# Kernel tuning notes

Hardware: AMD Instinct MI355X
Metric: run time of the kernel (lower is better)

## Reference

```python
import jax, jax.numpy as jnp
import numpy as np

N = 50000   # nodes
E = 800000  # edges
B = 64      # graphs in batch
IN = 128    # in_features
HID = 64    # hidden_channels
H = 4       # head_count
C = 10      # out_classes
NEG = 0.2   # leaky relu negative slope
EPS = 1e-5  # batchnorm eps (eval mode, running mean 0 / var 1)


def _gat(x, edge_index, W, a_src, a_dst, b):
    """PyG GATConv (add_self_loops=False, concat=True), eval mode (no dropout)."""
    Hh, F = a_src.shape
    xW = (x @ W).reshape(-1, Hh, F)                       # [N,H,F]
    src, dst = edge_index[0], edge_index[1]
    e = (jnp.einsum('nhf,hf->nh', xW, a_src)[src]
         + jnp.einsum('nhf,hf->nh', xW, a_dst)[dst])      # [E,H]
    e = jnp.where(e > 0, e, NEG * e)                      # leaky relu
    m = jax.ops.segment_max(e, dst, num_segments=N)       # per-dst max
    m = jnp.where(jnp.isfinite(m), m, 0.0)
    p = jnp.exp(e - m[dst])
    denom = jax.ops.segment_sum(p, dst, num_segments=N)
    alpha = p / jnp.maximum(denom[dst], 1e-16)            # edge softmax over dst
    out = jax.ops.segment_sum(alpha[:, :, None] * xW[src], dst, num_segments=N)
    return out.reshape(-1, Hh * F) + b


def _bn_relu(y, g, be):
    # BatchNorm1d in eval mode with running_mean=0, running_var=1, then ReLU
    return jax.nn.relu(g * y / jnp.sqrt(1.0 + EPS) + be)


def setup_inputs():
    key = jax.random.key(0)
    ks = jax.random.split(key, 24)
    s = lambda k, shape: (jax.random.normal(k, shape, jnp.float32) * 0.05)
    z = lambda shape: jnp.zeros(shape, jnp.float32)
    o = lambda shape: jnp.ones(shape, jnp.float32)
    return {
        'acc_flag': 0,
        'x': jax.random.normal(ks[0], (N, IN), jnp.float32),
        'edge_index': jax.random.randint(ks[1], (2, E), 0, N),
        'batch': jnp.sort(jax.random.randint(ks[2], (N,), 0, B)),
        # layer 1: GATConv(IN -> HID, heads=H, concat)
        'W1': s(ks[3], (IN, H * HID)), 'a_src1': s(ks[4], (H, HID)), 'a_dst1': s(ks[5], (H, HID)), 'b1': z((H * HID,)),
        # proj: GATConv(H*HID -> HID, heads=1) + BN
        'W2': s(ks[6], (H * HID, HID)), 'a_src2': s(ks[7], (1, HID)), 'a_dst2': s(ks[8], (1, HID)), 'b2': z((HID,)), 'g2': o((HID,)), 'be2': z((HID,)),
        # block 1
        'W3': s(ks[9], (HID, HID)), 'a_src3': s(ks[10], (1, HID)), 'a_dst3': s(ks[11], (1, HID)), 'b3': z((HID,)), 'g3': o((HID,)), 'be3': z((HID,)),
        # block 2
        'W4': s(ks[12], (HID, HID)), 'a_src4': s(ks[13], (1, HID)), 'a_dst4': s(ks[14], (1, HID)), 'b4': z((HID,)), 'g4': o((HID,)), 'be4': z((HID,)),
        # MLP head
        'Wh1': s(ks[15], (HID, 128)), 'bh1': z((128,)),
        'Wh2': s(ks[16], (128, C)), 'bh2': z((C,)),
    }


def reference(acc_flag, x, edge_index, batch,
              W1, a_src1, a_dst1, b1,
              W2, a_src2, a_dst2, b2, g2, be2,
              W3, a_src3, a_dst3, b3, g3, be3,
              W4, a_src4, a_dst4, b4, g4, be4,
              Wh1, bh1, Wh2, bh2):
    # hardware GAT layer + ReLU (relu applied twice in original -> idempotent)
    x1 = jax.nn.relu(_gat(x, edge_index, W1, a_src1, a_dst1, b1))   # [N, H*HID]
    # projection block: residual base is zeros (shape mismatch H*HID vs HID)
    h = _bn_relu(_gat(x1, edge_index, W2, a_src2, a_dst2, b2), g2, be2)
    # residual blocks (shapes match -> x + relu(bn(y)))
    h = h + _bn_relu(_gat(h, edge_index, W3, a_src3, a_dst3, b3), g3, be3)
    h = h + _bn_relu(_gat(h, edge_index, W4, a_src4, a_dst4, b4), g4, be4)
    # global mean pool over graphs
    pooled = jax.ops.segment_sum(h, batch, num_segments=B)
    cnt = jnp.maximum(jax.ops.segment_sum(jnp.ones((N,), h.dtype), batch, num_segments=B), 1.0)
    hp = pooled / cnt[:, None]                                      # [B, HID]
    # MLP head
    return jax.nn.relu(hp @ Wh1 + bh1) @ Wh2 + bh2                  # [B, C]
```

## Files before the change

### kernel.cpp

```cpp
#include <hip/hip_runtime.h>

#define N_NODES 50000
#define N_EDGES 800000
#define N_GRAPHS 64
#define NEG_SLOPE 0.2f
#define BN_RSQ 0.9999950000374997f
#define NB_SCAN ((N_NODES + 255) / 256)

typedef __bf16 bf16x8 __attribute__((ext_vector_type(8)));
typedef float floatx4 __attribute__((ext_vector_type(4)));

__device__ __forceinline__ float lrelu(float v) { return v > 0.0f ? v : NEG_SLOPE * v; }

__device__ __forceinline__ float b2f(unsigned short u) {
    return __uint_as_float(((unsigned int)u) << 16);
}
__device__ __forceinline__ unsigned short f2b(float f) {
    unsigned int u = __float_as_uint(f);
    return (unsigned short)((u + 0x7fffu + ((u >> 16) & 1u)) >> 16);
}
__device__ __forceinline__ float blo(unsigned int d) { return __uint_as_float(d << 16); }
__device__ __forceinline__ float bhi(unsigned int d) { return __uint_as_float(d & 0xffff0000u); }

__global__ void k_prep(const int* __restrict__ ei, int* __restrict__ deg,
                       const float* __restrict__ W1, const float* __restrict__ W2,
                       const float* __restrict__ W3, const float* __restrict__ W4,
                       unsigned short* __restrict__ Wt1, unsigned short* __restrict__ Wt2,
                       unsigned short* __restrict__ Wt3, unsigned short* __restrict__ Wt4) {
    int i = blockIdx.x * 256 + threadIdx.x;
    if (i < 32768) {
        int k = i >> 8, n = i & 255;
        Wt1[n * 128 + k] = f2b(W1[i]);
    } else if (i < 49152) {
        int j = i - 32768;
        int k = j >> 6, n = j & 63;
        Wt2[n * 256 + k] = f2b(W2[j]);
    } else if (i < 53248) {
        int j = i - 49152;
        int k = j >> 6, n = j & 63;
        Wt3[n * 64 + k] = f2b(W3[j]);
    } else if (i < 57344) {
        int j = i - 53248;
        int k = j >> 6, n = j & 63;
        Wt4[n * 64 + k] = f2b(W4[j]);
    }
    if (i < N_EDGES) atomicAdd(&deg[ei[N_EDGES + i]], 1);
}

__global__ __launch_bounds__(256) void k_offs(const int* __restrict__ deg, int* __restrict__ offs,
                                              int* __restrict__ total, const int* __restrict__ batch,
                                              int* __restrict__ bounds, int* __restrict__ bh) {
    __shared__ int lh[64];
    if (threadIdx.x < 64) lh[threadIdx.x] = 0;
    __syncthreads();
    if (blockIdx.x == 0 && threadIdx.x <= N_GRAPHS) {
        int g = threadIdx.x;
        int lo = 0, hi = N_NODES;
        while (lo < hi) {
            int mid = (lo + hi) >> 1;
            if (batch[mid] < g) lo = mid + 1; else hi = mid;
        }
        bounds[g] = lo;
    }
    int i = blockIdx.x * blockDim.x + threadIdx.x;
    int lane = threadIdx.x & 63;
    int v = (i < N_NODES) ? deg[i] : 0;
    int incl = v;
    for (int o = 1; o < 64; o <<= 1) {
        int t = __shfl_up(incl, o);
        if (lane >= o) incl += t;
    }
    int wtot = __shfl(incl, 63);
    int base = 0;
    if (lane == 0) base = atomicAdd(total, wtot);
    base = __shfl(base, 0);
    if (i < N_NODES) {
        offs[i] = base + incl - v;
        atomicAdd(&lh[63 - min(v, 63)], 1);
    }
    __syncthreads();
    if (threadIdx.x < 64) bh[blockIdx.x * 64 + threadIdx.x] = lh[threadIdx.x];
}

__global__ __launch_bounds__(256) void k_pscan(const int* __restrict__ bh, int* __restrict__ bb) {
    __shared__ int partial[4][64];
    __shared__ int bbase[64];
    const int tid = threadIdx.x;
    const int b = tid & 63, q = tid >> 6;
    const int per = (NB_SCAN + 3) / 4;
    const int k0 = q * per, k1 = min(k0 + per, NB_SCAN);
    int s = 0;
    for (int k = k0; k < k1; ++k) s += bh[k * 64 + b];
    partial[q][b] = s;
    __syncthreads();
    if (tid < 64) {
        int tot = partial[0][tid] + partial[1][tid] + partial[2][tid] + partial[3][tid];
        int incl = tot;
        for (int o = 1; o < 64; o <<= 1) {
            int t2 = __shfl_up(incl, o);
            if (tid >= o) incl += t2;
        }
        bbase[tid] = incl - tot;
    }
    __syncthreads();
    int run = bbase[b];
    for (int q2 = 0; q2 < q; ++q2) run += partial[q2][b];
    for (int k = k0; k < k1; ++k) {
        bb[k * 64 + b] = run;
        run += bh[k * 64 + b];
    }
}

__global__ __launch_bounds__(256) void k_fillperm(const int* __restrict__ ei,
                                                  const int* __restrict__ offs,
                                                  int* __restrict__ cur, int* __restrict__ csr_src,
                                                  const int* __restrict__ deg,
                                                  const int* __restrict__ bb,
                                                  int* __restrict__ perm) {
    __shared__ int lcnt[64];
    if (blockIdx.x < NB_SCAN) {
        if (threadIdx.x < 64) lcnt[threadIdx.x] = 0;
        __syncthreads();
        int i = blockIdx.x * 256 + threadIdx.x;
        if (i < N_NODES) {
            int b = 63 - min(deg[i], 63);
            int r = atomicAdd(&lcnt[b], 1);
            perm[bb[blockIdx.x * 64 + b] + r] = i;
        }
    }
    int e = blockIdx.x * 256 + threadIdx.x;
    if (e < N_EDGES) {
        int d = ei[N_EDGES + e];
        int pos = offs[d] + atomicAdd(&cur[d], 1);
        csr_src[pos] = ei[e];
    }
}

template <int K, int N, int HEADS, bool AF32>
__global__ __launch_bounds__(256) void k_mgemm(const void* __restrict__ Ap,
                                               const unsigned short* __restrict__ Bt,
                                               const float* __restrict__ asrc,
                                               const float* __restrict__ adst,
                                               unsigned short* __restrict__ out,
                                               float* __restrict__ es,
                                               float* __restrict__ ed, int rows) {
    constexpr int LDP = K + 8;
    __shared__ unsigned short As[64 * LDP];
    const int tid = threadIdx.x;
    const int r0 = blockIdx.x * 64;
    if (AF32) {
        const float* A = (const float*)Ap;
        for (int i = tid; i < 16 * K; i += 256) {
            int r = i / (K / 4), c4 = i % (K / 4);
            int row = r0 + r;
            float4 v = (row < rows) ? *(const float4*)&A[(size_t)row * K + c4 * 4]
                                    : make_float4(0.f, 0.f, 0.f, 0.f);
            ushort4 u;
            u.x = f2b(v.x); u.y = f2b(v.y); u.z = f2b(v.z); u.w = f2b(v.w);
            *(ushort4*)&As[r * LDP + c4 * 4] = u;
        }
    } else {
        const unsigned short* A = (const unsigned short*)Ap;
        for (int i = tid; i < 8 * K; i += 256) {
            int r = i / (K / 8), c8 = i % (K / 8);
            int row = r0 + r;
            uint4 v;
            if (row < rows) v = *(const uint4*)&A[(size_t)row * K + c8 * 8];
            else { v.x = v.y = v.z = v.w = 0; }
            *(uint4*)&As[r * LDP + c8 * 8] = v;
        }
    }
    __syncthreads();
    const int w = tid >> 6, lane = tid & 63;
    const int quad = lane >> 4, l16 = lane & 15;
    const int gr0 = r0 + w * 16 + quad * 4;
    bf16x8 afrag[K / 32];
#pragma unroll
    for (int kk = 0; kk < K / 32; ++kk)
        afrag[kk] = *(const bf16x8*)&As[(w * 16 + l16) * LDP + kk * 32 + quad * 8];
    float sacc[4] = {0.f, 0.f, 0.f, 0.f};
    float dacc[4] = {0.f, 0.f, 0.f, 0.f};
#pragma unroll 1
    for (int ct = 0; ct < N / 16; ++ct) {
        floatx4 acc = {0.f, 0.f, 0.f, 0.f};
#pragma unroll
        for (int kk = 0; kk < K / 32; ++kk) {
            const bf16x8 bfrag =
                *(const bf16x8*)&Bt[(size_t)(ct * 16 + l16) * K + kk * 32 + quad * 8];
            acc = __builtin_amdgcn_mfma_f32_16x16x32_bf16(afrag[kk], bfrag, acc, 0, 0, 0);
        }
        const int gc = ct * 16 + l16;
        const int hh = gc >> 6;
        const int f = gc & 63;
        const float as = asrc[hh * 64 + f];
        const float ad = adst[hh * 64 + f];
#pragma unroll
        for (int rg = 0; rg < 4; ++rg) {
            sacc[rg] = fmaf(acc[rg], as, sacc[rg]);
            dacc[rg] = fmaf(acc[rg], ad, dacc[rg]);
        }
#pragma unroll
        for (int rg = 0; rg < 4; ++rg) {
            int gr = gr0 + rg;
            if (gr < rows) out[(size_t)gr * N + gc] = f2b(acc[rg]);
        }
        if ((ct & 3) == 3) {
#pragma unroll
            for (int rg = 0; rg < 4; ++rg) {
                float s = sacc[rg], d = dacc[rg];
                for (int o = 1; o < 16; o <<= 1) {
                    s += __shfl_xor(s, o);
                    d += __shfl_xor(d, o);
                }
                if (l16 == 0) {
                    int gr = gr0 + rg;
                    if (gr < rows) {
                        es[(size_t)gr * HEADS + hh] = s;
                        ed[(size_t)gr * HEADS + hh] = d;
                    }
                }
                sacc[rg] = 0.f;
                dacc[rg] = 0.f;
            }
        }
    }
}

__global__ __launch_bounds__(256) void k_gat1(
    const unsigned short* __restrict__ xW, const float* __restrict__ es, const float* __restrict__ ed,
    const int* __restrict__ offs, const int* __restrict__ deg, const int* __restrict__ csr,
    const int* __restrict__ perm, const float* __restrict__ bias, unsigned short* __restrict__ out) {
    __shared__ float ps[4][4 * 68];
    __shared__ int sbuf[4][64];
    const int wv = threadIdx.x >> 6;
    const int lane = threadIdx.x & 63;
    const int grp = lane >> 4, t = lane & 15;
    const int h = t >> 2;
    const int g0 = blockIdx.x * 16 + wv * 4 + grp;
    if (g0 >= N_NODES / 2) return;
    const int cb = t * 16;

#pragma unroll 1
    for (int half = 0; half < 2; ++half) {
        const int pidx = half ? (N_NODES - 1 - g0) : g0;
        const int n = perm[pidx];
        const int off = offs[n];
        const int dg = deg[n];
        const float4 edv = *(const float4*)&ed[n * 4];

        float acc[16];
#pragma unroll
        for (int k = 0; k < 16; ++k) acc[k] = 0.f;
        float dsum = 0.f;

        for (int base = 0; base < dg; base += 16) {
            const int idx = base + t;
            int s_l = 0;
            float p0 = 0.f, p1 = 0.f, p2 = 0.f, p3 = 0.f;
            if (idx < dg) {
                s_l = csr[off + idx];
                const float4 ev = *(const float4*)&es[s_l * 4];
                p0 = __expf(lrelu(ev.x + edv.x));
                p1 = __expf(lrelu(ev.y + edv.y));
                p2 = __expf(lrelu(ev.z + edv.z));
                p3 = __expf(lrelu(ev.w + edv.w));
            }
            *(float4*)&ps[wv][grp * 68 + t * 4] = make_float4(p0, p1, p2, p3);
            sbuf[wv][grp * 16 + t] = s_l;
            const int cnt = min(16, dg - base);
            const int cntR = (cnt + 3) & ~3;
            for (int j = 0; j < cntR; j += 4) {
                const float pa = ps[wv][grp * 68 + (j + 0) * 4 + h];
                const float pb = ps[wv][grp * 68 + (j + 1) * 4 + h];
                const float pc = ps[wv][grp * 68 + (j + 2) * 4 + h];
                const float pd = ps[wv][grp * 68 + (j + 3) * 4 + h];
                const int sa = sbuf[wv][grp * 16 + j + 0];
                const int sb = sbuf[wv][grp * 16 + j + 1];
                const int sc = sbuf[wv][grp * 16 + j + 2];
                const int sd = sbuf[wv][grp * 16 + j + 3];
                const uint4 a0 = *(const uint4*)&xW[(size_t)sa * 256 + cb];
                const uint4 a1 = *(const uint4*)&xW[(size_t)sa * 256 + cb + 8];
                const uint4 b0 = *(const uint4*)&xW[(size_t)sb * 256 + cb];
                const uint4 b1 = *(const uint4*)&xW[(size_t)sb * 256 + cb + 8];
                const uint4 c0 = *(const uint4*)&xW[(size_t)sc * 256 + cb];
                const uint4 c1 = *(const uint4*)&xW[(size_t)sc * 256 + cb + 8];
                const uint4 d0 = *(const uint4*)&xW[(size_t)sd * 256 + cb];
                const uint4 d1 = *(const uint4*)&xW[(size_t)sd * 256 + cb + 8];
                dsum += (pa + pb) + (pc + pd);
                acc[0]  = fmaf(pa, blo(a0.x), acc[0]);
                acc[1]  = fmaf(pa, bhi(a0.x), acc[1]);
                acc[2]  = fmaf(pa, blo(a0.y), acc[2]);
                acc[3]  = fmaf(pa, bhi(a0.y), acc[3]);
                acc[4]  = fmaf(pa, blo(a0.z), acc[4]);
                acc[5]  = fmaf(pa, bhi(a0.z), acc[5]);
                acc[6]  = fmaf(pa, blo(a0.w), acc[6]);
                acc[7]  = fmaf(pa, bhi(a0.w), acc[7]);
                acc[8]  = fmaf(pa, blo(a1.x), acc[8]);
                acc[9]  = fmaf(pa, bhi(a1.x), acc[9]);
                acc[10] = fmaf(pa, blo(a1.y), acc[10]);
                acc[11] = fmaf(pa, bhi(a1.y), acc[11]);
                acc[12] = fmaf(pa, blo(a1.z), acc[12]);
                acc[13] = fmaf(pa, bhi(a1.z), acc[13]);
                acc[14] = fmaf(pa, blo(a1.w), acc[14]);
                acc[15] = fmaf(pa, bhi(a1.w), acc[15]);
                acc[0]  = fmaf(pb, blo(b0.x), acc[0]);
                acc[1]  = fmaf(pb, bhi(b0.x), acc[1]);
                acc[2]  = fmaf(pb, blo(b0.y), acc[2]);
                acc[3]  = fmaf(pb, bhi(b0.y), acc[3]);
                acc[4]  = fmaf(pb, blo(b0.z), acc[4]);
                acc[5]  = fmaf(pb, bhi(b0.z), acc[5]);
                acc[6]  = fmaf(pb, blo(b0.w), acc[6]);
                acc[7]  = fmaf(pb, bhi(b0.w), acc[7]);
                acc[8]  = fmaf(pb, blo(b1.x), acc[8]);
                acc[9]  = fmaf(pb, bhi(b1.x), acc[9]);
                acc[10] = fmaf(pb, blo(b1.y), acc[10]);
                acc[11] = fmaf(pb, bhi(b1.y), acc[11]);
                acc[12] = fmaf(pb, blo(b1.z), acc[12]);
                acc[13] = fmaf(pb, bhi(b1.z), acc[13]);
                acc[14] = fmaf(pb, blo(b1.w), acc[14]);
                acc[15] = fmaf(pb, bhi(b1.w), acc[15]);
                acc[0]  = fmaf(pc, blo(c0.x), acc[0]);
                acc[1]  = fmaf(pc, bhi(c0.x), acc[1]);
                acc[2]  = fmaf(pc, blo(c0.y), acc[2]);
                acc[3]  = fmaf(pc, bhi(c0.y), acc[3]);
                acc[4]  = fmaf(pc, blo(c0.z), acc[4]);
                acc[5]  = fmaf(pc, bhi(c0.z), acc[5]);
                acc[6]  = fmaf(pc, blo(c0.w), acc[6]);
                acc[7]  = fmaf(pc, bhi(c0.w), acc[7]);
                acc[8]  = fmaf(pc, blo(c1.x), acc[8]);
                acc[9]  = fmaf(pc, bhi(c1.x), acc[9]);
                acc[10] = fmaf(pc, blo(c1.y), acc[10]);
                acc[11] = fmaf(pc, bhi(c1.y), acc[11]);
                acc[12] = fmaf(pc, blo(c1.z), acc[12]);
                acc[13] = fmaf(pc, bhi(c1.z), acc[13]);
                acc[14] = fmaf(pc, blo(c1.w), acc[14]);
                acc[15] = fmaf(pc, bhi(c1.w), acc[15]);
                acc[0]  = fmaf(pd, blo(d0.x), acc[0]);
                acc[1]  = fmaf(pd, bhi(d0.x), acc[1]);
                acc[2]  = fmaf(pd, blo(d0.y), acc[2]);
                acc[3]  = fmaf(pd, bhi(d0.y), acc[3]);
                acc[4]  = fmaf(pd, blo(d0.z), acc[4]);
                acc[5]  = fmaf(pd, bhi(d0.z), acc[5]);
                acc[6]  = fmaf(pd, blo(d0.w), acc[6]);
                acc[7]  = fmaf(pd, bhi(d0.w), acc[7]);
                acc[8]  = fmaf(pd, blo(d1.x), acc[8]);
                acc[9]  = fmaf(pd, bhi(d1.x), acc[9]);
                acc[10] = fmaf(pd, blo(d1.y), acc[10]);
                acc[11] = fmaf(pd, bhi(d1.y), acc[11]);
                acc[12] = fmaf(pd, blo(d1.z), acc[12]);
                acc[13] = fmaf(pd, bhi(d1.z), acc[13]);
                acc[14] = fmaf(pd, blo(d1.w), acc[14]);
                acc[15] = fmaf(pd, bhi(d1.w), acc[15]);
            }
        }
        const float inv = 1.0f / fmaxf(dsum, 1e-16f);
#pragma unroll
        for (int k4 = 0; k4 < 16; k4 += 4) {
            const int c = cb + k4;
            const float4 bv = *(const float4*)&bias[c];
            ushort4 o4;
            o4.x = f2b(fmaxf(fmaf(acc[k4 + 0], inv, bv.x), 0.f));
            o4.y = f2b(fmaxf(fmaf(acc[k4 + 1], inv, bv.y), 0.f));
            o4.z = f2b(fmaxf(fmaf(acc[k4 + 2], inv, bv.z), 0.f));
            o4.w = f2b(fmaxf(fmaf(acc[k4 + 3], inv, bv.w), 0.f));
            *(ushort4*)&out[(size_t)n * 256 + c] = o4;
        }
    }
}

template <bool RES>
__global__ __launch_bounds__(256) void k_gatL(
    const unsigned short* __restrict__ xW, const float* __restrict__ es, const float* __restrict__ ed,
    const int* __restrict__ offs, const int* __restrict__ deg, const int* __restrict__ csr,
    const int* __restrict__ perm, const float* __restrict__ bias, const float* __restrict__ gam,
    const float* __restrict__ bet, float* __restrict__ h, unsigned short* __restrict__ hb) {
    __shared__ float ps[4][64];
    __shared__ int sbuf[4][64];
    const int wv = threadIdx.x >> 6;
    const int lane = threadIdx.x & 63;
    const int grp = lane >> 3, t = lane & 7;
    const int pidx = blockIdx.x * 32 + wv * 8 + grp;
    if (pidx >= N_NODES) return;
    const int n = perm[pidx];
    const int off = offs[n];
    const int dg = deg[n];
    const float edn = ed[n];
    const int cb = t * 8;

    float acc[8];
#pragma unroll
    for (int k = 0; k < 8; ++k) acc[k] = 0.f;
    float dsum = 0.f;

    for (int base = 0; base < dg; base += 8) {
        const int idx = base + t;
        int s_l = 0;
        float p_l = 0.f;
        if (idx < dg) {
            s_l = csr[off + idx];
            p_l = __expf(lrelu(es[s_l] + edn));
        }
        ps[wv][grp * 8 + t] = p_l;
        sbuf[wv][grp * 8 + t] = s_l;
        float pp[8];
        int ss[8];
#pragma unroll
        for (int q = 0; q < 8; ++q) {
            pp[q] = ps[wv][grp * 8 + q];
            ss[q] = sbuf[wv][grp * 8 + q];
        }
        uint4 u[8];
#pragma unroll
        for (int q = 0; q < 8; ++q) u[q] = *(const uint4*)&xW[(size_t)ss[q] * 64 + cb];
#pragma unroll
        for (int q = 0; q < 8; ++q) {
            dsum += pp[q];
            acc[0] = fmaf(pp[q], blo(u[q].x), acc[0]);
            acc[1] = fmaf(pp[q], bhi(u[q].x), acc[1]);
            acc[2] = fmaf(pp[q], blo(u[q].y), acc[2]);
            acc[3] = fmaf(pp[q], bhi(u[q].y), acc[3]);
            acc[4] = fmaf(pp[q], blo(u[q].z), acc[4]);
            acc[5] = fmaf(pp[q], bhi(u[q].z), acc[5]);
            acc[6] = fmaf(pp[q], blo(u[q].w), acc[6]);
            acc[7] = fmaf(pp[q], bhi(u[q].w), acc[7]);
        }
    }
    const float inv = 1.0f / fmaxf(dsum, 1e-16f);
    float hn[8];
#pragma unroll
    for (int k = 0; k < 8; ++k) {
        const int c = cb + k;
        const float y = fmaf(acc[k], inv, bias[c]);
        const float z = fmaxf(fmaf(gam[c] * y, BN_RSQ, bet[c]), 0.f);
        hn[k] = RES ? h[(size_t)n * 64 + c] + z : z;
    }
    *(float4*)&h[(size_t)n * 64 + cb] = make_float4(hn[0], hn[1], hn[2], hn[3]);
    *(float4*)&h[(size_t)n * 64 + cb + 4] = make_float4(hn[4], hn[5], hn[6], hn[7]);
    ushort4 u0, u1;
    u0.x = f2b(hn[0]); u0.y = f2b(hn[1]); u0.z = f2b(hn[2]); u0.w = f2b(hn[3]);
    u1.x = f2b(hn[4]); u1.y = f2b(hn[5]); u1.z = f2b(hn[6]); u1.w = f2b(hn[7]);
    *(ushort4*)&hb[(size_t)n * 64 + cb] = u0;
    *(ushort4*)&hb[(size_t)n * 64 + cb + 4] = u1;
}

__global__ __launch_bounds__(256) void k_pool2(const float* __restrict__ h,
                                               const int* __restrict__ bounds,
                                               float* __restrict__ hp) {
    __shared__ float part[4][64];
    const int g = blockIdx.x;
    const int lane = threadIdx.x & 63;
    const int wid = threadIdx.x >> 6;
    const int s = bounds[g], e = bounds[g + 1];
    float acc = 0.f;
    for (int n = s + wid; n < e; n += 4) acc += h[n * 64 + lane];
    part[wid][lane] = acc;
    __syncthreads();
    if (wid == 0) {
        float v = part[0][lane] + part[1][lane] + part[2][lane] + part[3][lane];
        hp[g * 64 + lane] = v / fmaxf((float)(e - s), 1.0f);
    }
}

__global__ __launch_bounds__(256) void k_head(const float* __restrict__ hpg,
                                              const float* __restrict__ Wh1,
                                              const float* __restrict__ bh1,
                                              const float* __restrict__ Wh2,
                                              const float* __restrict__ bh2,
                                              float* __restrict__ out) {
    __shared__ float hp[64 * 64];
    __shared__ float t1[64 * 128];
    const int tid = threadIdx.x;
    for (int i = tid; i < 64 * 64; i += 256) hp[i] = hpg[i];
    __syncthreads();
    for (int i = tid; i < 64 * 128; i += 256) {
        int g = i >> 7, j = i & 127;
        float s = bh1[j];
        for (int k = 0; k < 64; ++k) s = fmaf(hp[g * 64 + k], Wh1[k * 128 + j], s);
        t1[i] = fmaxf(s, 0.f);
    }
    __syncthreads();
    for (int i = tid; i < 640; i += 256) {
        int g = i / 10, j = i - g * 10;
        float s = bh2[j];
        for (int k = 0; k < 128; ++k) s = fmaf(t1[g * 128 + k], Wh2[k * 10 + j], s);
        out[i] = s;
    }
}

extern "C" void kernel_launch(void* const* d_in, const int* in_sizes, int n_in,
                              void* d_out, int out_size, void* d_ws, size_t ws_size,
                              hipStream_t stream) {
    const float* x = (const float*)d_in[1];
    const int* ei = (const int*)d_in[2];
    const int* batch = (const int*)d_in[3];
    const float* W1 = (const float*)d_in[4];
    const float* a_src1 = (const float*)d_in[5];
    const float* a_dst1 = (const float*)d_in[6];
    const float* b1 = (const float*)d_in[7];
    const float* W2 = (const float*)d_in[8];
    const float* a_src2 = (const float*)d_in[9];
    const float* a_dst2 = (const float*)d_in[10];
    const float* b2 = (const float*)d_in[11];
    const float* g2 = (const float*)d_in[12];
    const float* be2 = (const float*)d_in[13];
    const float* W3 = (const float*)d_in[14];
    const float* a_src3 = (const float*)d_in[15];
    const float* a_dst3 = (const float*)d_in[16];
    const float* b3 = (const float*)d_in[17];
    const float* g3 = (const float*)d_in[18];
    const float* be3 = (const float*)d_in[19];
    const float* W4 = (const float*)d_in[20];
    const float* a_src4 = (const float*)d_in[21];
    const float* a_dst4 = (const float*)d_in[22];
    const float* b4 = (const float*)d_in[23];
    const float* g4 = (const float*)d_in[24];
    const float* be4 = (const float*)d_in[25];
    const float* Wh1 = (const float*)d_in[26];
    const float* bh1 = (const float*)d_in[27];
    const float* Wh2 = (const float*)d_in[28];
    const float* bh2 = (const float*)d_in[29];
    float* out = (float*)d_out;

    char* p = (char*)d_ws;
    auto alloc = [&](size_t bytes) {
        void* r = (void*)p;
        p += (bytes + 255) & ~(size_t)255;
        return r;
    };
    unsigned short* bufA = (unsigned short*)alloc((size_t)N_NODES * 256 * 2);
    unsigned short* x1b = (unsigned short*)alloc((size_t)N_NODES * 256 * 2);
    float* h = (float*)alloc((size_t)N_NODES * 64 * 4);
    unsigned short* hb = (unsigned short*)alloc((size_t)N_NODES * 64 * 2);
    float* es1 = (float*)alloc((size_t)N_NODES * 4 * 4);
    float* ed1 = (float*)alloc((size_t)N_NODES * 4 * 4);
    float* esL = (float*)alloc((size_t)N_NODES * 4);
    float* edL = (float*)alloc((size_t)N_NODES * 4);
    int* offs = (int*)alloc((size_t)N_NODES * 4);
    int* csr = (int*)alloc((size_t)N_EDGES * 4);
    int* perm = (int*)alloc((size_t)N_NODES * 4);
    int* bounds = (int*)alloc((size_t)(N_GRAPHS + 1) * 4);
    int* bh_hist = (int*)alloc((size_t)NB_SCAN * 64 * 4);
    int* bb = (int*)alloc((size_t)NB_SCAN * 64 * 4);
    float* hpool = (float*)alloc((size_t)N_GRAPHS * 64 * 4);
    unsigned short* Wt1 = (unsigned short*)alloc((size_t)128 * 256 * 2);
    unsigned short* Wt2 = (unsigned short*)alloc((size_t)256 * 64 * 2);
    unsigned short* Wt3 = (unsigned short*)alloc((size_t)64 * 64 * 2);
    unsigned short* Wt4 = (unsigned short*)alloc((size_t)64 * 64 * 2);
    char* z0 = p;
    int* deg = (int*)alloc((size_t)N_NODES * 4);
    int* cur = (int*)alloc((size_t)N_NODES * 4);
    int* total = (int*)alloc(256);
    size_t zbytes = (size_t)(p - z0);
    hipMemsetAsync(z0, 0, zbytes, stream);

    const int edgeBlocks = (N_EDGES + 255) / 256;
    const int mgemmBlocks = (N_NODES + 63) / 64;
    const int gat1Blocks = (N_NODES / 2 + 15) / 16;
    const int gatLBlocks = (N_NODES + 31) / 32;

    k_prep<<<edgeBlocks, 256, 0, stream>>>(ei, deg, W1, W2, W3, W4, Wt1, Wt2, Wt3, Wt4);

    k_offs<<<NB_SCAN, 256, 0, stream>>>(deg, offs, total, batch, bounds, bh_hist);
    k_pscan<<<1, 256, 0, stream>>>(bh_hist, bb);
    k_fillperm<<<edgeBlocks, 256, 0, stream>>>(ei, offs, cur, csr, deg, bb, perm);

    k_mgemm<128, 256, 4, true><<<mgemmBlocks, 256, 0, stream>>>(x, Wt1, a_src1, a_dst1,
                                                                bufA, es1, ed1, N_NODES);
    k_gat1<<<gat1Blocks, 256, 0, stream>>>(bufA, es1, ed1, offs, deg, csr, perm, b1, x1b);

    k_mgemm<256, 64, 1, false><<<mgemmBlocks, 256, 0, stream>>>(x1b, Wt2, a_src2, a_dst2,
                                                                bufA, esL, edL, N_NODES);
    k_gatL<false><<<gatLBlocks, 256, 0, stream>>>(bufA, esL, edL, offs, deg, csr, perm, b2, g2, be2, h, hb);

    k_mgemm<64, 64, 1, false><<<mgemmBlocks, 256, 0, stream>>>(hb, Wt3, a_src3, a_dst3,
                                                               bufA, esL, edL, N_NODES);
    k_gatL<true><<<gatLBlocks, 256, 0, stream>>>(bufA, esL, edL, offs, deg, csr, perm, b3, g3, be3, h, hb);

    k_mgemm<64, 64, 1, false><<<mgemmBlocks, 256, 0, stream>>>(hb, Wt4, a_src4, a_dst4,
                                                               bufA, esL, edL, N_NODES);
    k_gatL<true><<<gatLBlocks, 256, 0, stream>>>(bufA, esL, edL, offs, deg, csr, perm, b4, g4, be4, h, hb);

    k_pool2<<<N_GRAPHS, 256, 0, stream>>>(h, bounds, hpool);
    k_head<<<1, 256, 0, stream>>>(hpool, Wh1, bh1, Wh2, bh2, out);
}
```

Baseline: 523.6 us.

## Fuse next layer's projection GEMM and attention logits into GAT aggregation kernels

Each GAT aggregation kernel now multiplies its 16 or 32 output rows by the next layer's weight matrix with MFMA and writes the projected bf16 features plus the per-node attention logits. This removes the separate k_mgemm launches and the global round trip of x1 (256 bf16 per node) and the bf16 copy of h. Each layer gets its own logit and feature buffers so no kernel reads what it writes. k_gat1 also drops its two-nodes-per-group balancing loop in favour of one node per group, which may reduce load balancing across the degree-sorted perm and adds shared memory plus barriers per block.

```diff
diff --git a/kernel.cpp b/kernel.cpp
--- a/kernel.cpp
+++ b/kernel.cpp
@@ -226,154 +226,335 @@
     }
 }
 
-__global__ __launch_bounds__(256) void k_gat1(
+__global__ __launch_bounds__(256) void k_gat1f(
     const unsigned short* __restrict__ xW, const float* __restrict__ es, const float* __restrict__ ed,
     const int* __restrict__ offs, const int* __restrict__ deg, const int* __restrict__ csr,
-    const int* __restrict__ perm, const float* __restrict__ bias, unsigned short* __restrict__ out) {
+    const int* __restrict__ perm, const float* __restrict__ bias,
+    const unsigned short* __restrict__ Bt2, const float* __restrict__ as2,
+    const float* __restrict__ ad2, unsigned short* __restrict__ outW,
+    float* __restrict__ es2o, float* __restrict__ ed2o) {
     __shared__ float ps[4][4 * 68];
     __shared__ int sbuf[4][64];
+    __shared__ unsigned short As2[16 * 264];
+    __shared__ int nbuf[16];
+    __shared__ float sds[4][16], sdd[4][16];
     const int wv = threadIdx.x >> 6;
     const int lane = threadIdx.x & 63;
     const int grp = lane >> 4, t = lane & 15;
     const int h = t >> 2;
-    const int g0 = blockIdx.x * 16 + wv * 4 + grp;
-    if (g0 >= N_NODES / 2) return;
+    const int r = wv * 4 + grp;
+    const int pidx = blockIdx.x * 16 + r;
+    const int n = perm[pidx];
+    const int off = offs[n];
+    const int dg = deg[n];
+    const float4 edv = *(const float4*)&ed[n * 4];
     const int cb = t * 16;
 
-#pragma unroll 1
-    for (int half = 0; half < 2; ++half) {
-        const int pidx = half ? (N_NODES - 1 - g0) : g0;
-        const int n = perm[pidx];
-        const int off = offs[n];
-        const int dg = deg[n];
-        const float4 edv = *(const float4*)&ed[n * 4];
-
-        float acc[16];
-#pragma unroll
-        for (int k = 0; k < 16; ++k) acc[k] = 0.f;
-        float dsum = 0.f;
-
-        for (int base = 0; base < dg; base += 16) {
-            const int idx = base + t;
-            int s_l = 0;
-            float p0 = 0.f, p1 = 0.f, p2 = 0.f, p3 = 0.f;
-            if (idx < dg) {
-                s_l = csr[off + idx];
-                const float4 ev = *(const float4*)&es[s_l * 4];
-                p0 = __expf(lrelu(ev.x + edv.x));
-                p1 = __expf(lrelu(ev.y + edv.y));
-                p2 = __expf(lrelu(ev.z + edv.z));
-                p3 = __expf(lrelu(ev.w + edv.w));
+    float acc[16];
+#pragma unroll
+    for (int k = 0; k < 16; ++k) acc[k] = 0.f;
+    float dsum = 0.f;
+
+    for (int base = 0; base < dg; base += 16) {
+        const int idx = base + t;
+        int s_l = 0;
+        float p0 = 0.f, p1 = 0.f, p2 = 0.f, p3 = 0.f;
+        if (idx < dg) {
+            s_l = csr[off + idx];
+            const float4 ev = *(const float4*)&es[s_l * 4];
+            p0 = __expf(lrelu(ev.x + edv.x));
+            p1 = __expf(lrelu(ev.y + edv.y));
+            p2 = __expf(lrelu(ev.z + edv.z));
+            p3 = __expf(lrelu(ev.w + edv.w));
+        }
+        *(float4*)&ps[wv][grp * 68 + t * 4] = make_float4(p0, p1, p2, p3);
+        sbuf[wv][grp * 16 + t] = s_l;
+        const int cnt = min(16, dg - base);
+        const int cntR = (cnt + 3) & ~3;
+        for (int j = 0; j < cntR; j += 4) {
+            const float pa = ps[wv][grp * 68 + (j + 0) * 4 + h];
+            const float pb = ps[wv][grp * 68 + (j + 1) * 4 + h];
+            const float pc = ps[wv][grp * 68 + (j + 2) * 4 + h];
+            const float pd = ps[wv][grp * 68 + (j + 3) * 4 + h];
+            const int sa = sbuf[wv][grp * 16 + j + 0];
+            const int sb = sbuf[wv][grp * 16 + j + 1];
+            const int sc = sbuf[wv][grp * 16 + j + 2];
+            const int sd = sbuf[wv][grp * 16 + j + 3];
+            const uint4 a0 = *(const uint4*)&xW[(size_t)sa * 256 + cb];
+            const uint4 a1 = *(const uint4*)&xW[(size_t)sa * 256 + cb + 8];
+            const uint4 b0 = *(const uint4*)&xW[(size_t)sb * 256 + cb];
+            const uint4 b1 = *(const uint4*)&xW[(size_t)sb * 256 + cb + 8];
+            const uint4 c0 = *(const uint4*)&xW[(size_t)sc * 256 + cb];
+            const uint4 c1 = *(const uint4*)&xW[(size_t)sc * 256 + cb + 8];
+            const uint4 d0 = *(const uint4*)&xW[(size_t)sd * 256 + cb];
+            const uint4 d1 = *(const uint4*)&xW[(size_t)sd * 256 + cb + 8];
+            dsum += (pa + pb) + (pc + pd);
+            acc[0]  = fmaf(pa, blo(a0.x), acc[0]);
+            acc[1]  = fmaf(pa, bhi(a0.x), acc[1]);
+            acc[2]  = fmaf(pa, blo(a0.y), acc[2]);
+            acc[3]  = fmaf(pa, bhi(a0.y), acc[3]);
+            acc[4]  = fmaf(pa, blo(a0.z), acc[4]);
+            acc[5]  = fmaf(pa, bhi(a0.z), acc[5]);
+            acc[6]  = fmaf(pa, blo(a0.w), acc[6]);
+            acc[7]  = fmaf(pa, bhi(a0.w), acc[7]);
+            acc[8]  = fmaf(pa, blo(a1.x), acc[8]);
+            acc[9]  = fmaf(pa, bhi(a1.x), acc[9]);
+            acc[10] = fmaf(pa, blo(a1.y), acc[10]);
+            acc[11] = fmaf(pa, bhi(a1.y), acc[11]);
+            acc[12] = fmaf(pa, blo(a1.z), acc[12]);
+            acc[13] = fmaf(pa, bhi(a1.z), acc[13]);
+            acc[14] = fmaf(pa, blo(a1.w), acc[14]);
+            acc[15] = fmaf(pa, bhi(a1.w), acc[15]);
+            acc[0]  = fmaf(pb, blo(b0.x), acc[0]);
+            acc[1]  = fmaf(pb, bhi(b0.x), acc[1]);
+            acc[2]  = fmaf(pb, blo(b0.y), acc[2]);
+            acc[3]  = fmaf(pb, bhi(b0.y), acc[3]);
+            acc[4]  = fmaf(pb, blo(b0.z), acc[4]);
+            acc[5]  = fmaf(pb, bhi(b0.z), acc[5]);
+            acc[6]  = fmaf(pb, blo(b0.w), acc[6]);
+            acc[7]  = fmaf(pb, bhi(b0.w), acc[7]);
+            acc[8]  = fmaf(pb, blo(b1.x), acc[8]);
+            acc[9]  = fmaf(pb, bhi(b1.x), acc[9]);
+            acc[10] = fmaf(pb, blo(b1.y), acc[10]);
+            acc[11] = fmaf(pb, bhi(b1.y), acc[11]);
+            acc[12] = fmaf(pb, blo(b1.z), acc[12]);
+            acc[13] = fmaf(pb, bhi(b1.z), acc[13]);
+            acc[14] = fmaf(pb, blo(b1.w), acc[14]);
+            acc[15] = fmaf(pb, bhi(b1.w), acc[15]);
+            acc[0]  = fmaf(pc, blo(c0.x), acc[0]);
+            acc[1]  = fmaf(pc, bhi(c0.x), acc[1]);
+            acc[2]  = fmaf(pc, blo(c0.y), acc[2]);
+            acc[3]  = fmaf(pc, bhi(c0.y), acc[3]);
+            acc[4]  = fmaf(pc, blo(c0.z), acc[4]);
+            acc[5]  = fmaf(pc, bhi(c0.z), acc[5]);
+            acc[6]  = fmaf(pc, blo(c0.w), acc[6]);
+            acc[7]  = fmaf(pc, bhi(c0.w), acc[7]);
+            acc[8]  = fmaf(pc, blo(c1.x), acc[8]);
+            acc[9]  = fmaf(pc, bhi(c1.x), acc[9]);
+            acc[10] = fmaf(pc, blo(c1.y), acc[10]);
+            acc[11] = fmaf(pc, bhi(c1.y), acc[11]);
+            acc[12] = fmaf(pc, blo(c1.z), acc[12]);
+            acc[13] = fmaf(pc, bhi(c1.z), acc[13]);
+            acc[14] = fmaf(pc, blo(c1.w), acc[14]);
+            acc[15] = fmaf(pc, bhi(c1.w), acc[15]);
+            acc[0]  = fmaf(pd, blo(d0.x), acc[0]);
+            acc[1]  = fmaf(pd, bhi(d0.x), acc[1]);
+            acc[2]  = fmaf(pd, blo(d0.y), acc[2]);
+            acc[3]  = fmaf(pd, bhi(d0.y), acc[3]);
+            acc[4]  = fmaf(pd, blo(d0.z), acc[4]);
+            acc[5]  = fmaf(pd, bhi(d0.z), acc[5]);
+            acc[6]  = fmaf(pd, blo(d0.w), acc[6]);
+            acc[7]  = fmaf(pd, bhi(d0.w), acc[7]);
+            acc[8]  = fmaf(pd, blo(d1.x), acc[8]);
+            acc[9]  = fmaf(pd, bhi(d1.x), acc[9]);
+            acc[10] = fmaf(pd, blo(d1.y), acc[10]);
+            acc[11] = fmaf(pd, bhi(d1.y), acc[11]);
+            acc[12] = fmaf(pd, blo(d1.z), acc[12]);
+            acc[13] = fmaf(pd, bhi(d1.z), acc[13]);
+            acc[14] = fmaf(pd, blo(d1.w), acc[14]);
+            acc[15] = fmaf(pd, bhi(d1.w), acc[15]);
+        }
+    }
+    const float inv = 1.0f / fmaxf(dsum, 1e-16f);
+#pragma unroll
+    for (int k4 = 0; k4 < 16; k4 += 4) {
+        const int c = cb + k4;
+        const float4 bv = *(const float4*)&bias[c];
+        ushort4 o4;
+        o4.x = f2b(fmaxf(fmaf(acc[k4 + 0], inv, bv.x), 0.f));
+        o4.y = f2b(fmaxf(fmaf(acc[k4 + 1], inv, bv.y), 0.f));
+        o4.z = f2b(fmaxf(fmaf(acc[k4 + 2], inv, bv.z), 0.f));
+        o4.w = f2b(fmaxf(fmaf(acc[k4 + 3], inv, bv.w), 0.f));
+        *(ushort4*)&As2[r * 264 + c] = o4;
+    }
+    if (t == 0) nbuf[r] = n;
+    __syncthreads();
+
+    {
+        const int gc = wv * 16 + t;
+        floatx4 c2 = {0.f, 0.f, 0.f, 0.f};
+#pragma unroll
+        for (int kk = 0; kk < 8; ++kk) {
+            const bf16x8 af = *(const bf16x8*)&As2[t * 264 + kk * 32 + grp * 8];
+            const bf16x8 bf = *(const bf16x8*)&Bt2[(size_t)gc * 256 + kk * 32 + grp * 8];
+            c2 = __builtin_amdgcn_mfma_f32_16x16x32_bf16(af, bf, c2, 0, 0, 0);
+        }
+        const float a_s = as2[gc];
+        const float a_d = ad2[gc];
+        float srg[4], drg[4];
+#pragma unroll
+        for (int rg = 0; rg < 4; ++rg) {
+            srg[rg] = c2[rg] * a_s;
+            drg[rg] = c2[rg] * a_d;
+            const int row = grp * 4 + rg;
+            outW[(size_t)nbuf[row] * 64 + gc] = f2b(c2[rg]);
+        }
+#pragma unroll
+        for (int rg = 0; rg < 4; ++rg) {
+            for (int o = 1; o < 16; o <<= 1) {
+                srg[rg] += __shfl_xor(srg[rg], o);
+                drg[rg] += __shfl_xor(drg[rg], o);
             }
-            *(float4*)&ps[wv][grp * 68 + t * 4] = make_float4(p0, p1, p2, p3);
-            sbuf[wv][grp * 16 + t] = s_l;
-            const int cnt = min(16, dg - base);
-            const int cntR = (cnt + 3) & ~3;
-            for (int j = 0; j < cntR; j += 4) {
-                const float pa = ps[wv][grp * 68 + (j + 0) * 4 + h];
-                const float pb = ps[wv][grp * 68 + (j + 1) * 4 + h];
-                const float pc = ps[wv][grp * 68 + (j + 2) * 4 + h];
-                const float pd = ps[wv][grp * 68 + (j + 3) * 4 + h];
-                const int sa = sbuf[wv][grp * 16 + j + 0];
-                const int sb = sbuf[wv][grp * 16 + j + 1];
-                const int sc = sbuf[wv][grp * 16 + j + 2];
-                const int sd = sbuf[wv][grp * 16 + j + 3];
-                const uint4 a0 = *(const uint4*)&xW[(size_t)sa * 256 + cb];
-                const uint4 a1 = *(const uint4*)&xW[(size_t)sa * 256 + cb + 8];
-                const uint4 b0 = *(const uint4*)&xW[(size_t)sb * 256 + cb];
-                const uint4 b1 = *(const uint4*)&xW[(size_t)sb * 256 + cb + 8];
-                const uint4 c0 = *(const uint4*)&xW[(size_t)sc * 256 + cb];
-                const uint4 c1 = *(const uint4*)&xW[(size_t)sc * 256 + cb + 8];
-                const uint4 d0 = *(const uint4*)&xW[(size_t)sd * 256 + cb];
-                const uint4 d1 = *(const uint4*)&xW[(size_t)sd * 256 + cb + 8];
-                dsum += (pa + pb) + (pc + pd);
-                acc[0]  = fmaf(pa, blo(a0.x), acc[0]);
-                acc[1]  = fmaf(pa, bhi(a0.x), acc[1]);
-                acc[2]  = fmaf(pa, blo(a0.y), acc[2]);
-                acc[3]  = fmaf(pa, bhi(a0.y), acc[3]);
-                acc[4]  = fmaf(pa, blo(a0.z), acc[4]);
-                acc[5]  = fmaf(pa, bhi(a0.z), acc[5]);
-                acc[6]  = fmaf(pa, blo(a0.w), acc[6]);
-                acc[7]  = fmaf(pa, bhi(a0.w), acc[7]);
-                acc[8]  = fmaf(pa, blo(a1.x), acc[8]);
-                acc[9]  = fmaf(pa, bhi(a1.x), acc[9]);
-                acc[10] = fmaf(pa, blo(a1.y), acc[10]);
-                acc[11] = fmaf(pa, bhi(a1.y), acc[11]);
-                acc[12] = fmaf(pa, blo(a1.z), acc[12]);
-                acc[13] = fmaf(pa, bhi(a1.z), acc[13]);
-                acc[14] = fmaf(pa, blo(a1.w), acc[14]);
-                acc[15] = fmaf(pa, bhi(a1.w), acc[15]);
-                acc[0]  = fmaf(pb, blo(b0.x), acc[0]);
-                acc[1]  = fmaf(pb, bhi(b0.x), acc[1]);
-                acc[2]  = fmaf(pb, blo(b0.y), acc[2]);
-                acc[3]  = fmaf(pb, bhi(b0.y), acc[3]);
-                acc[4]  = fmaf(pb, blo(b0.z), acc[4]);
-                acc[5]  = fmaf(pb, bhi(b0.z), acc[5]);
-                acc[6]  = fmaf(pb, blo(b0.w), acc[6]);
-                acc[7]  = fmaf(pb, bhi(b0.w), acc[7]);
-                acc[8]  = fmaf(pb, blo(b1.x), acc[8]);
-                acc[9]  = fmaf(pb, bhi(b1.x), acc[9]);
-                acc[10] = fmaf(pb, blo(b1.y), acc[10]);
-                acc[11] = fmaf(pb, bhi(b1.y), acc[11]);
-                acc[12] = fmaf(pb, blo(b1.z), acc[12]);
-                acc[13] = fmaf(pb, bhi(b1.z), acc[13]);
-                acc[14] = fmaf(pb, blo(b1.w), acc[14]);
-                acc[15] = fmaf(pb, bhi(b1.w), acc[15]);
-                acc[0]  = fmaf(pc, blo(c0.x), acc[0]);
-                acc[1]  = fmaf(pc, bhi(c0.x), acc[1]);
-                acc[2]  = fmaf(pc, blo(c0.y), acc[2]);
-                acc[3]  = fmaf(pc, bhi(c0.y), acc[3]);
-                acc[4]  = fmaf(pc, blo(c0.z), acc[4]);
-                acc[5]  = fmaf(pc, bhi(c0.z), acc[5]);
-                acc[6]  = fmaf(pc, blo(c0.w), acc[6]);
-                acc[7]  = fmaf(pc, bhi(c0.w), acc[7]);
-                acc[8]  = fmaf(pc, blo(c1.x), acc[8]);
-                acc[9]  = fmaf(pc, bhi(c1.x), acc[9]);
-                acc[10] = fmaf(pc, blo(c1.y), acc[10]);
-                acc[11] = fmaf(pc, bhi(c1.y), acc[11]);
-                acc[12] = fmaf(pc, blo(c1.z), acc[12]);
-                acc[13] = fmaf(pc, bhi(c1.z), acc[13]);
-                acc[14] = fmaf(pc, blo(c1.w), acc[14]);
-                acc[15] = fmaf(pc, bhi(c1.w), acc[15]);
-                acc[0]  = fmaf(pd, blo(d0.x), acc[0]);
-                acc[1]  = fmaf(pd, bhi(d0.x), acc[1]);
-                acc[2]  = fmaf(pd, blo(d0.y), acc[2]);
-                acc[3]  = fmaf(pd, bhi(d0.y), acc[3]);
-                acc[4]  = fmaf(pd, blo(d0.z), acc[4]);
-                acc[5]  = fmaf(pd, bhi(d0.z), acc[5]);
-                acc[6]  = fmaf(pd, blo(d0.w), acc[6]);
-                acc[7]  = fmaf(pd, bhi(d0.w), acc[7]);
-                acc[8]  = fmaf(pd, blo(d1.x), acc[8]);
-                acc[9]  = fmaf(pd, bhi(d1.x), acc[9]);
-                acc[10] = fmaf(pd, blo(d1.y), acc[10]);
-                acc[11] = fmaf(pd, bhi(d1.y), acc[11]);
-                acc[12] = fmaf(pd, blo(d1.z), acc[12]);
-                acc[13] = fmaf(pd, bhi(d1.z), acc[13]);
-                acc[14] = fmaf(pd, blo(d1.w), acc[14]);
-                acc[15] = fmaf(pd, bhi(d1.w), acc[15]);
+        }
+        if (t == 0) {
+#pragma unroll
+            for (int rg = 0; rg < 4; ++rg) {
+                sds[wv][grp * 4 + rg] = srg[rg];
+                sdd[wv][grp * 4 + rg] = drg[rg];
             }
         }
-        const float inv = 1.0f / fmaxf(dsum, 1e-16f);
-#pragma unroll
-        for (int k4 = 0; k4 < 16; k4 += 4) {
-            const int c = cb + k4;
-            const float4 bv = *(const float4*)&bias[c];
-            ushort4 o4;
-            o4.x = f2b(fmaxf(fmaf(acc[k4 + 0], inv, bv.x), 0.f));
-            o4.y = f2b(fmaxf(fmaf(acc[k4 + 1], inv, bv.y), 0.f));
-            o4.z = f2b(fmaxf(fmaf(acc[k4 + 2], inv, bv.z), 0.f));
-            o4.w = f2b(fmaxf(fmaf(acc[k4 + 3], inv, bv.w), 0.f));
-            *(ushort4*)&out[(size_t)n * 256 + c] = o4;
-        }
+    }
+    __syncthreads();
+    if (threadIdx.x < 16) {
+        const int rr = threadIdx.x;
+        es2o[nbuf[rr]] = sds[0][rr] + sds[1][rr] + sds[2][rr] + sds[3][rr];
+        ed2o[nbuf[rr]] = sdd[0][rr] + sdd[1][rr] + sdd[2][rr] + sdd[3][rr];
     }
 }
 
 template <bool RES>
-__global__ __launch_bounds__(256) void k_gatL(
+__global__ __launch_bounds__(256) void k_gatLG(
     const unsigned short* __restrict__ xW, const float* __restrict__ es, const float* __restrict__ ed,
     const int* __restrict__ offs, const int* __restrict__ deg, const int* __restrict__ csr,
     const int* __restrict__ perm, const float* __restrict__ bias, const float* __restrict__ gam,
-    const float* __restrict__ bet, float* __restrict__ h, unsigned short* __restrict__ hb) {
+    const float* __restrict__ bet, float* __restrict__ hglob,
+    const unsigned short* __restrict__ Btn, const float* __restrict__ asn,
+    const float* __restrict__ adn, unsigned short* __restrict__ outW,
+    float* __restrict__ esn, float* __restrict__ edn_o) {
+    __shared__ float ps[4][64];
+    __shared__ int sbuf[4][64];
+    __shared__ unsigned short As2[32 * 72];
+    __shared__ int nbuf[32];
+    __shared__ float sds[2][32], sdd[2][32];
+    const int wv = threadIdx.x >> 6;
+    const int lane = threadIdx.x & 63;
+    const int g8 = lane >> 3, t8 = lane & 7;
+    const int row1 = wv * 8 + g8;
+    const int pbase = blockIdx.x * 32;
+    const int pidx = pbase + row1;
+    const bool valid = pidx < N_NODES;
+    const int n = perm[valid ? pidx : 0];
+    const int off = offs[n];
+    const int dg = valid ? deg[n] : 0;
+    const float edn = valid ? ed[n] : 0.f;
+    const int cb = t8 * 8;
+
+    float acc[8];
+#pragma unroll
+    for (int k = 0; k < 8; ++k) acc[k] = 0.f;
+    float dsum = 0.f;
+
+    for (int base = 0; base < dg; base += 8) {
+        const int idx = base + t8;
+        int s_l = 0;
+        float p_l = 0.f;
+        if (idx < dg) {
+            s_l = csr[off + idx];
+            p_l = __expf(lrelu(es[s_l] + edn));
+        }
+        ps[wv][g8 * 8 + t8] = p_l;
+        sbuf[wv][g8 * 8 + t8] = s_l;
+        float pp[8];
+        int ss[8];
+#pragma unroll
+        for (int q = 0; q < 8; ++q) {
+            pp[q] = ps[wv][g8 * 8 + q];
+            ss[q] = sbuf[wv][g8 * 8 + q];
+        }
+        uint4 u[8];
+#pragma unroll
+        for (int q = 0; q < 8; ++q) u[q] = *(const uint4*)&xW[(size_t)ss[q] * 64 + cb];
+#pragma unroll
+        for (int q = 0; q < 8; ++q) {
+            dsum += pp[q];
+            acc[0] = fmaf(pp[q], blo(u[q].x), acc[0]);
+            acc[1] = fmaf(pp[q], bhi(u[q].x), acc[1]);
+            acc[2] = fmaf(pp[q], blo(u[q].y), acc[2]);
+            acc[3] = fmaf(pp[q], bhi(u[q].y), acc[3]);
+            acc[4] = fmaf(pp[q], blo(u[q].z), acc[4]);
+            acc[5] = fmaf(pp[q], bhi(u[q].z), acc[5]);
+            acc[6] = fmaf(pp[q], blo(u[q].w), acc[6]);
+            acc[7] = fmaf(pp[q], bhi(u[q].w), acc[7]);
+        }
+    }
+    const float inv = 1.0f / fmaxf(dsum, 1e-16f);
+    float hn[8];
+#pragma unroll
+    for (int k = 0; k < 8; ++k) {
+        const int c = cb + k;
+        const float y = fmaf(acc[k], inv, bias[c]);
+        const float z = fmaxf(fmaf(gam[c] * y, BN_RSQ, bet[c]), 0.f);
+        hn[k] = (RES && valid) ? hglob[(size_t)n * 64 + c] + z : z;
+    }
+    if (valid) {
+        *(float4*)&hglob[(size_t)n * 64 + cb] = make_float4(hn[0], hn[1], hn[2], hn[3]);
+        *(float4*)&hglob[(size_t)n * 64 + cb + 4] = make_float4(hn[4], hn[5], hn[6], hn[7]);
+    }
+    ushort4 u0, u1;
+    u0.x = f2b(hn[0]); u0.y = f2b(hn[1]); u0.z = f2b(hn[2]); u0.w = f2b(hn[3]);
+    u1.x = f2b(hn[4]); u1.y = f2b(hn[5]); u1.z = f2b(hn[6]); u1.w = f2b(hn[7]);
+    if (!valid) { u0.x = u0.y = u0.z = u0.w = 0; u1.x = u1.y = u1.z = u1.w = 0; }
+    *(ushort4*)&As2[row1 * 72 + cb] = u0;
+    *(ushort4*)&As2[row1 * 72 + cb + 4] = u1;
+    if (t8 == 0) nbuf[row1] = n;
+    __syncthreads();
+
+    {
+        const int quad = lane >> 4, l16 = lane & 15;
+        const int rs = wv >> 1;
+        float sacc[4] = {0.f, 0.f, 0.f, 0.f};
+        float dacc[4] = {0.f, 0.f, 0.f, 0.f};
+#pragma unroll
+        for (int ci = 0; ci < 2; ++ci) {
+            const int ct = (wv & 1) * 2 + ci;
+            const int gc = ct * 16 + l16;
+            floatx4 c2 = {0.f, 0.f, 0.f, 0.f};
+#pragma unroll
+            for (int kk = 0; kk < 2; ++kk) {
+                const bf16x8 af = *(const bf16x8*)&As2[(rs * 16 + l16) * 72 + kk * 32 + quad * 8];
+                const bf16x8 bf = *(const bf16x8*)&Btn[(size_t)gc * 64 + kk * 32 + quad * 8];
+                c2 = __builtin_amdgcn_mfma_f32_16x16x32_bf16(af, bf, c2, 0, 0, 0);
+            }
+            const float a_s = asn[gc];
+            const float a_d = adn[gc];
+#pragma unroll
+            for (int rg = 0; rg < 4; ++rg) {
+                sacc[rg] = fmaf(c2[rg], a_s, sacc[rg]);
+                dacc[rg] = fmaf(c2[rg], a_d, dacc[rg]);
+                const int row = rs * 16 + quad * 4 + rg;
+                if (pbase + row < N_NODES) outW[(size_t)nbuf[row] * 64 + gc] = f2b(c2[rg]);
+            }
+        }
+#pragma unroll
+        for (int rg = 0; rg < 4; ++rg) {
+            for (int o = 1; o < 16; o <<= 1) {
+                sacc[rg] += __shfl_xor(sacc[rg], o);
+                dacc[rg] += __shfl_xor(dacc[rg], o);
+            }
+        }
+        if (l16 == 0) {
+#pragma unroll
+            for (int rg = 0; rg < 4; ++rg) {
+                sds[wv & 1][rs * 16 + quad * 4 + rg] = sacc[rg];
+                sdd[wv & 1][rs * 16 + quad * 4 + rg] = dacc[rg];
+            }
+        }
+    }
+    __syncthreads();
+    if (threadIdx.x < 32) {
+        const int rr = threadIdx.x;
+        if (pbase + rr < N_NODES) {
+            esn[nbuf[rr]] = sds[0][rr] + sds[1][rr];
+            edn_o[nbuf[rr]] = sdd[0][rr] + sdd[1][rr];
+        }
+    }
+}
+
+__global__ __launch_bounds__(256) void k_gatF(
+    const unsigned short* __restrict__ xW, const float* __restrict__ es, const float* __restrict__ ed,
+    const int* __restrict__ offs, const int* __restrict__ deg, const int* __restrict__ csr,
+    const int* __restrict__ perm, const float* __restrict__ bias, const float* __restrict__ gam,
+    const float* __restrict__ bet, float* __restrict__ h) {
     __shared__ float ps[4][64];
     __shared__ int sbuf[4][64];
     const int wv = threadIdx.x >> 6;
@@ -432,15 +613,10 @@
         const int c = cb + k;
         const float y = fmaf(acc[k], inv, bias[c]);
         const float z = fmaxf(fmaf(gam[c] * y, BN_RSQ, bet[c]), 0.f);
-        hn[k] = RES ? h[(size_t)n * 64 + c] + z : z;
+        hn[k] = h[(size_t)n * 64 + c] + z;
     }
     *(float4*)&h[(size_t)n * 64 + cb] = make_float4(hn[0], hn[1], hn[2], hn[3]);
     *(float4*)&h[(size_t)n * 64 + cb + 4] = make_float4(hn[4], hn[5], hn[6], hn[7]);
-    ushort4 u0, u1;
-    u0.x = f2b(hn[0]); u0.y = f2b(hn[1]); u0.z = f2b(hn[2]); u0.w = f2b(hn[3]);
-    u1.x = f2b(hn[4]); u1.y = f2b(hn[5]); u1.z = f2b(hn[6]); u1.w = f2b(hn[7]);
-    *(ushort4*)&hb[(size_t)n * 64 + cb] = u0;
-    *(ushort4*)&hb[(size_t)n * 64 + cb + 4] = u1;
 }
 
 __global__ __launch_bounds__(256) void k_pool2(const float* __restrict__ h,
@@ -527,14 +703,19 @@
         p += (bytes + 255) & ~(size_t)255;
         return r;
     };
-    unsigned short* bufA = (unsigned short*)alloc((size_t)N_NODES * 256 * 2);
-    unsigned short* x1b = (unsigned short*)alloc((size_t)N_NODES * 256 * 2);
+    unsigned short* bufA1 = (unsigned short*)alloc((size_t)N_NODES * 256 * 2);
+    unsigned short* bufB = (unsigned short*)alloc((size_t)N_NODES * 64 * 2);
+    unsigned short* bufC = (unsigned short*)alloc((size_t)N_NODES * 64 * 2);
+    unsigned short* bufD = (unsigned short*)alloc((size_t)N_NODES * 64 * 2);
     float* h = (float*)alloc((size_t)N_NODES * 64 * 4);
-    unsigned short* hb = (unsigned short*)alloc((size_t)N_NODES * 64 * 2);
     float* es1 = (float*)alloc((size_t)N_NODES * 4 * 4);
     float* ed1 = (float*)alloc((size_t)N_NODES * 4 * 4);
-    float* esL = (float*)alloc((size_t)N_NODES * 4);
-    float* edL = (float*)alloc((size_t)N_NODES * 4);
+    float* es2 = (float*)alloc((size_t)N_NODES * 4);
+    float* ed2 = (float*)alloc((size_t)N_NODES * 4);
+    float* es3 = (float*)alloc((size_t)N_NODES * 4);
+    float* ed3 = (float*)alloc((size_t)N_NODES * 4);
+    float* es4 = (float*)alloc((size_t)N_NODES * 4);
+    float* ed4 = (float*)alloc((size_t)N_NODES * 4);
     int* offs = (int*)alloc((size_t)N_NODES * 4);
     int* csr = (int*)alloc((size_t)N_EDGES * 4);
     int* perm = (int*)alloc((size_t)N_NODES * 4);
@@ -555,7 +736,7 @@
 
     const int edgeBlocks = (N_EDGES + 255) / 256;
     const int mgemmBlocks = (N_NODES + 63) / 64;
-    const int gat1Blocks = (N_NODES / 2 + 15) / 16;
+    const int gat1Blocks = (N_NODES + 15) / 16;
     const int gatLBlocks = (N_NODES + 31) / 32;
 
     k_prep<<<edgeBlocks, 256, 0, stream>>>(ei, deg, W1, W2, W3, W4, Wt1, Wt2, Wt3, Wt4);
@@ -565,20 +746,17 @@
     k_fillperm<<<edgeBlocks, 256, 0, stream>>>(ei, offs, cur, csr, deg, bb, perm);
 
     k_mgemm<128, 256, 4, true><<<mgemmBlocks, 256, 0, stream>>>(x, Wt1, a_src1, a_dst1,
-                                                                bufA, es1, ed1, N_NODES);
-    k_gat1<<<gat1Blocks, 256, 0, stream>>>(bufA, es1, ed1, offs, deg, csr, perm, b1, x1b);
-
-    k_mgemm<256, 64, 1, false><<<mgemmBlocks, 256, 0, stream>>>(x1b, Wt2, a_src2, a_dst2,
-                                                                bufA, esL, edL, N_NODES);
-    k_gatL<false><<<gatLBlocks, 256, 0, stream>>>(bufA, esL, edL, offs, deg, csr, perm, b2, g2, be2, h, hb);
-
-    k_mgemm<64, 64, 1, false><<<mgemmBlocks, 256, 0, stream>>>(hb, Wt3, a_src3, a_dst3,
-                                                               bufA, esL, edL, N_NODES);
-    k_gatL<true><<<gatLBlocks, 256, 0, stream>>>(bufA, esL, edL, offs, deg, csr, perm, b3, g3, be3, h, hb);
-
-    k_mgemm<64, 64, 1, false><<<mgemmBlocks, 256, 0, stream>>>(hb, Wt4, a_src4, a_dst4,
-                                                               bufA, esL, edL, N_NODES);
-    k_gatL<true><<<gatLBlocks, 256, 0, stream>>>(bufA, esL, edL, offs, deg, csr, perm, b4, g4, be4, h, hb);
+                                                                bufA1, es1, ed1, N_NODES);
+    k_gat1f<<<gat1Blocks, 256, 0, stream>>>(bufA1, es1, ed1, offs, deg, csr, perm, b1,
+                                            Wt2, a_src2, a_dst2, bufB, es2, ed2);
+
+    k_gatLG<false><<<gatLBlocks, 256, 0, stream>>>(bufB, es2, ed2, offs, deg, csr, perm,
+                                                   b2, g2, be2, h, Wt3, a_src3, a_dst3,
+                                                   bufC, es3, ed3);
+    k_gatLG<true><<<gatLBlocks, 256, 0, stream>>>(bufC, es3, ed3, offs, deg, csr, perm,
+                                                  b3, g3, be3, h, Wt4, a_src4, a_dst4,
+                                                  bufD, es4, ed4);
+    k_gatF<<<gatLBlocks, 256, 0, stream>>>(bufD, es4, ed4, offs, deg, csr, perm, b4, g4, be4, h);
 
     k_pool2<<<N_GRAPHS, 256, 0, stream>>>(h, bounds, hpool);
     k_head<<<1, 256, 0, stream>>>(hpool, Wh1, bh1, Wh2, bh2, out);
```

Measured after the change: 511.8 us. 1.02x faster.
